# Kernel tuning notes

Hardware: AMD Instinct MI355X
Metric: run time of the kernel (lower is better)

Reference implementation:

```python
import jax, jax.numpy as jnp
import numpy as np

B, N_PATCH, DIM, HEADS = 64, 196, 768, 12
WIN = (14, 14)
NUM_REL_DIST = (2 * WIN[0] - 1) * (2 * WIN[1] - 1) + 3  # 732


def _build_rel_pos_index():
    ch, cw = np.arange(WIN[0]), np.arange(WIN[1])
    coords = np.stack(np.meshgrid(ch, cw, indexing='ij'))  # (2, Wh, Ww)
    flat = coords.reshape(2, -1)  # (2, Wh*Ww)
    rel = flat[:, :, None] - flat[:, None, :]  # (2, N, N)
    rel = rel.transpose(1, 2, 0).astype(np.int64)  # (N, N, 2)
    rel[:, :, 0] += WIN[0] - 1
    rel[:, :, 1] += WIN[1] - 1
    rel[:, :, 0] *= 2 * WIN[1] - 1
    n = WIN[0] * WIN[1] + 1
    idx = np.zeros((n, n), dtype=np.int64)
    idx[1:, 1:] = rel.sum(-1)
    idx[0, 0:] = NUM_REL_DIST - 3
    idx[0:, 0] = NUM_REL_DIST - 2
    idx[0, 0] = NUM_REL_DIST - 1
    return jnp.asarray(idx)


def setup_inputs() -> dict:
    key = jax.random.key(0)
    ks = jax.random.split(key, 6)
    d = DIM
    return {
        'x': jax.random.normal(ks[0], (B, N_PATCH + 1, d), dtype=jnp.float32),
        'qkv_w': jax.random.normal(ks[1], (3 * d, d), dtype=jnp.float32) * (d ** -0.5),
        'q_bias': jnp.zeros((d,), dtype=jnp.float32),
        'v_bias': jnp.zeros((d,), dtype=jnp.float32),
        'rpb_table': jax.random.normal(ks[2], (NUM_REL_DIST, HEADS), dtype=jnp.float32) * 0.02,
        'proj_w': jax.random.normal(ks[3], (d, d), dtype=jnp.float32) * (d ** -0.5),
        'proj_b': jnp.zeros((d,), dtype=jnp.float32),
        'rel_pos_index': _build_rel_pos_index(),
    }


def reference(x, qkv_w, q_bias, v_bias, rpb_table, proj_w, proj_b, rel_pos_index):
    Bn, N, C = x.shape
    H = HEADS
    hd = C // H
    scale = hd ** -0.5
    bias = jnp.concatenate([q_bias, jnp.zeros_like(v_bias), v_bias])
    qkv = x @ qkv_w.T + bias  # (B, N, 3C)
    qkv = qkv.reshape(Bn, N, 3, H, hd).transpose(2, 0, 3, 1, 4)  # (3, B, H, N, hd)
    q, k, v = qkv[0] * scale, qkv[1], qkv[2]
    attn = jnp.einsum('bhnd,bhmd->bhnm', q, k)  # (B, H, N, N)
    rpb = rpb_table[rel_pos_index.reshape(-1)].reshape(N, N, H).transpose(2, 0, 1)
    attn = jax.nn.softmax(attn + rpb[None], axis=-1)
    out = jnp.einsum('bhnm,bhmd->bhnd', attn, v)  # (B, H, N, hd)
    out = out.transpose(0, 2, 1, 3).reshape(Bn, N, C)
    return out @ proj_w.T + proj_b
```

## Files before the change

### kernel.cpp

```cpp
#include <hip/hip_runtime.h>
#include <hip/hip_bf16.h>

#define HEADS   12
#define HD      64
#define NTOK    197
#define BATCH   64
#define M_TOK   (BATCH*NTOK)
#define DIMC    768
#define NPAIR   (NTOK*NTOK)
#define MPAD    224

typedef __attribute__((ext_vector_type(8))) short bf16x8;
typedef __attribute__((ext_vector_type(4))) short s16x4;
typedef __attribute__((ext_vector_type(4))) float f32x4;

static __device__ __forceinline__ short f2bf(float f) {
    unsigned u = __float_as_uint(f);
    unsigned r = (u + 0x7FFFu + ((u >> 16) & 1u)) >> 16;
    return (short)r;
}

#define NX (M_TOK * DIMC)
#define NW (3 * DIMC * DIMC)
#define NP (DIMC * DIMC)
__global__ void cvt_kernel(const float* __restrict__ s0, short* __restrict__ d0,
                           const float* __restrict__ s1, short* __restrict__ d1,
                           const float* __restrict__ s2, short* __restrict__ d2) {
    int i = (blockIdx.x * 256 + threadIdx.x) * 4;
    const float* s; short* d;
    if (i < NX)                { s = s0 + i; d = d0 + i; }
    else if (i < NX + NW)      { s = s1 + (i - NX); d = d1 + (i - NX); }
    else if (i < NX + NW + NP) { s = s2 + (i - NX - NW); d = d2 + (i - NX - NW); }
    else return;
    const float4 v = *(const float4*)s;
    s16x4 b; b[0] = f2bf(v.x); b[1] = f2bf(v.y); b[2] = f2bf(v.z); b[3] = f2bf(v.w);
    *(s16x4*)d = b;
}

__global__ void rpb_kernel(const float* __restrict__ table,
                           const int* __restrict__ idx,
                           float* __restrict__ rpb_full) {
    int i = blockIdx.x * 256 + threadIdx.x;
    if (i >= NPAIR) return;
    int id = idx[i];
    #pragma unroll
    for (int h = 0; h < HEADS; ++h)
        rpb_full[(size_t)h * NPAIR + i] = table[id * HEADS + h];
}

#define STAGE(LA, LB, kt)                                                       \
    _Pragma("unroll")                                                           \
    for (int i = 0; i < 4; ++i) {                                               \
        __builtin_amdgcn_global_load_lds(                                       \
            (const __attribute__((address_space(1))) void*)(aptr[i] + (kt) * 64),\
            (__attribute__((address_space(3))) void*)&(LA)[(wv * 4 + i) * 512], \
            16, 0, 0);                                                          \
        __builtin_amdgcn_global_load_lds(                                       \
            (const __attribute__((address_space(1))) void*)(bptr[i] + (kt) * 64),\
            (__attribute__((address_space(3))) void*)&(LB)[(wv * 4 + i) * 512], \
            16, 0, 0);                                                          \
    }

#define COMPUTE(LA, LB)                                                         \
    _Pragma("unroll")                                                           \
    for (int ks = 0; ks < 2; ++ks) {                                            \
        bf16x8 af[4], bfr[4];                                                   \
        const int kk = (((ks * 4 + g) ^ (c16 & 7)) << 3);    \
        _Pragma("unroll")                                                       \
        for (int i = 0; i < 4; ++i)                                             \
            af[i] = *(const bf16x8*)&(LA)[(wr * 64 + i * 16 + c16) * 64 + kk];  \
        _Pragma("unroll")                                                       \
        for (int j = 0; j < 4; ++j)                                             \
            bfr[j] = *(const bf16x8*)&(LB)[(wc * 64 + j * 16 + c16) * 64 + kk]; \
        _Pragma("unroll")                                                       \
        for (int i = 0; i < 4; ++i)                                             \
            _Pragma("unroll")                                                   \
            for (int j = 0; j < 4; ++j)                                         \
                acc[i][j] = __builtin_amdgcn_mfma_f32_16x16x32_bf16(            \
                    af[i], bfr[j], acc[i][j], 0, 0, 0);                         \
    }

__global__ __launch_bounds__(256) void qkv_gemm_kernel(
    const short* __restrict__ xb, const short* __restrict__ wb,
    const float* __restrict__ qb, const float* __restrict__ vb,
    short* __restrict__ q_ws, short* __restrict__ k_ws,
    short* __restrict__ vt_ws) {
    __shared__ __align__(16) short lds_a0[128 * 64];
    __shared__ __align__(16) short lds_a1[128 * 64];
    __shared__ __align__(16) short lds_bb[2 * 128 * 64];
    const int tid  = threadIdx.x;
    const int lane = tid & 63;
    const int wv   = tid >> 6;
    const int wr   = wv >> 1, wc = wv & 1;
    const int flat = blockIdx.x;
    const int xcd  = flat & 7, pos = flat >> 3;
    const int swz  = ((xcd < 6) ? xcd * 223 : 1338 + (xcd - 6) * 222) + pos;
    const int bm   = swz / 18, bn = swz - bm * 18;
    const int g    = lane >> 4, c16 = lane & 15;

    f32x4 acc[4][4] = {};

    const int lrow = lane >> 3;
    const int lcol = ((lane & 7) ^ lrow) * 8;
    const short* aptr[4];
    const short* bptr[4];
    #pragma unroll
    for (int i = 0; i < 4; ++i) {
        const int r  = (wv * 4 + i) * 8 + lrow;
        int gr = bm * 128 + r; if (gr > M_TOK - 1) gr = M_TOK - 1;
        aptr[i] = xb + (size_t)gr * DIMC + lcol;
        bptr[i] = wb + (size_t)(bn * 128 + r) * DIMC + lcol;
    }

    STAGE(lds_a0, lds_bb, 0);
    __syncthreads();
    #pragma unroll
    for (int kp = 0; kp < 6; ++kp) {
        STAGE(lds_a1, (lds_bb + 8192), 2 * kp + 1);
        COMPUTE(lds_a0, lds_bb);
        __syncthreads();
        if (kp < 5) { STAGE(lds_a0, lds_bb, 2 * kp + 2); }
        COMPUTE(lds_a1, (lds_bb + 8192));
        if (kp < 5) __syncthreads();
    }

    __syncthreads();
    short* t = lds_bb;
    if (bn < 12) {
        const int isq = (bn < 6);
        #pragma unroll
        for (int j = 0; j < 4; ++j) {
            const int col = wc * 64 + j * 16 + c16;
            const int r   = isq ? bn * 128 + col : bn * 128 + col - DIMC;
            const float bias = isq ? qb[r] : 0.0f;
            #pragma unroll
            for (int i = 0; i < 4; ++i) {
                const int tok0 = wr * 64 + i * 16 + (g << 2);
                #pragma unroll
                for (int rg = 0; rg < 4; ++rg) {
                    const int tok = tok0 + rg;
                    const int sw  = ((tok >> 2) & 3) << 4;
                    float val = acc[i][j][rg];
                    if (isq) val = (val + bias) * 0.125f;
                    t[tok * 128 + (col ^ sw)] = f2bf(val);
                }
            }
        }
        __syncthreads();
        short* dst = isq ? q_ws : k_ws;
        const int rbase = isq ? bn * 128 : bn * 128 - DIMC;
        for (int tr = 0; tr < 32; ++tr) {
            const int tok = wv * 32 + tr;
            const int tt  = bm * 128 + tok;
            if (tt >= M_TOK) continue;
            const int bb = tt / NTOK, nn = tt - bb * NTOK;
            const int sw = ((tok >> 2) & 3) << 4;
            #pragma unroll
            for (int half = 0; half < 2; ++half) {
                const int col = half * 64 + lane;
                const int h   = (rbase + half * 64) >> 6;
                dst[(((size_t)bb * HEADS + h) * NTOK + nn) * HD + lane] =
                    t[tok * 128 + (col ^ sw)];
            }
        }
    } else {
        #pragma unroll
        for (int i = 0; i < 4; ++i) {
            const int lt0 = wr * 64 + i * 16 + (g << 2);
            #pragma unroll
            for (int j = 0; j < 4; ++j) {
                const int col  = wc * 64 + j * 16 + c16;
                const int sw   = (col & 7) << 3;
                const float bias = vb[(bn - 12) * 128 + col];
                #pragma unroll
                for (int rg = 0; rg < 4; ++rg)
                    t[col * 128 + ((lt0 + rg) ^ sw)] = f2bf(acc[i][j][rg] + bias);
            }
        }
        __syncthreads();
        for (int cc = 0; cc < 32; ++cc) {
            const int col = cc * 4 + wv;
            const int sw  = (col & 7) << 3;
            const int r   = bn * 128 + col - 1536;
            const int h   = r >> 6, d = r & 63;
            #pragma unroll
            for (int half = 0; half < 2; ++half) {
                const int lt = lane + half * 64;
                const int tt = bm * 128 + lt;
                if (tt < M_TOK) {
                    const int b = tt / NTOK, n = tt - b * NTOK;
                    vt_ws[(((size_t)b * HEADS + h) * HD + d) * MPAD + n] =
                        t[col * 128 + (lt ^ sw)];
                }
            }
        }
    }
}

__global__ __launch_bounds__(64) void attn_kernel(
    const short* __restrict__ q_ws, const short* __restrict__ k_ws,
    const short* __restrict__ vt_ws, const float* __restrict__ rpb_full,
    short* __restrict__ o_ws) {
    __shared__ __align__(16) short p_lds[16 * 232];
    const int lane = threadIdx.x;
    const int id   = blockIdx.x;
    const int slot = id & 7;
    const int rest = id >> 3;
    const int rt   = rest % 13;
    const int bh   = (rest / 13) * 8 + slot;
    const int b    = bh / HEADS, h = bh - b * HEADS;
    const int g    = lane >> 4, c16 = lane & 15;

    bf16x8 qa0, qa1;
    {
        const size_t base = ((size_t)bh * NTOK + (rt * 16 + c16)) * HD + g * 8;
        qa0 = *(const bf16x8*)(q_ws + base);
        qa1 = *(const bf16x8*)(q_ws + base + 32);
    }

    bf16x8 kb0[14], kb1[14];
    #pragma unroll
    for (int mt = 0; mt < 14; ++mt) {
        const size_t base = ((size_t)bh * NTOK + (mt * 16 + c16)) * HD + g * 8;
        kb0[mt] = *(const bf16x8*)(k_ws + base);
        kb1[mt] = *(const bf16x8*)(k_ws + base + 32);
    }

    f32x4 sacc[14];
    #pragma unroll
    for (int t = 0; t < 14; ++t) sacc[t] = (f32x4){0.f, 0.f, 0.f, 0.f};
    #pragma unroll
    for (int mt = 0; mt < 14; ++mt) {
        sacc[mt] = __builtin_amdgcn_mfma_f32_16x16x32_bf16(qa0, kb0[mt], sacc[mt], 0, 0, 0);
        sacc[mt] = __builtin_amdgcn_mfma_f32_16x16x32_bf16(qa1, kb1[mt], sacc[mt], 0, 0, 0);
    }

    float rp[4][14];
    #pragma unroll
    for (int rg = 0; rg < 4; ++rg) {
        int n = rt * 16 + g * 4 + rg; int nc = n > NTOK - 1 ? NTOK - 1 : n;
        const float* rbase = rpb_full + (size_t)h * NPAIR + nc * NTOK;
        #pragma unroll
        for (int mt = 0; mt < 14; ++mt) {
            int m = mt * 16 + c16; int mc = m > NTOK - 1 ? NTOK - 1 : m;
            rp[rg][mt] = rbase[mc];
        }
    }

    float mx[4] = {-1e30f, -1e30f, -1e30f, -1e30f};
    #pragma unroll
    for (int rg = 0; rg < 4; ++rg) {
        const int n = rt * 16 + g * 4 + rg;
        #pragma unroll
        for (int mt = 0; mt < 14; ++mt) {
            const int m = mt * 16 + c16;
            float s = (n < NTOK && m < NTOK) ? sacc[mt][rg] + rp[rg][mt] : -1e30f;
            sacc[mt][rg] = s;
            mx[rg] = fmaxf(mx[rg], s);
        }
    }
    #pragma unroll
    for (int off = 1; off < 16; off <<= 1)
        #pragma unroll
        for (int rg = 0; rg < 4; ++rg)
            mx[rg] = fmaxf(mx[rg], __shfl_xor(mx[rg], off, 64));

    float sm[4] = {0.f, 0.f, 0.f, 0.f};
    #pragma unroll
    for (int mt = 0; mt < 14; ++mt)
        #pragma unroll
        for (int rg = 0; rg < 4; ++rg) {
            float p = exp2f((sacc[mt][rg] - mx[rg]) * 1.44269504f);
            sm[rg] += p;
            p_lds[(g * 4 + rg) * 232 + mt * 16 + c16] = f2bf(p);
        }

    bf16x8 vbf[7][4];
    #pragma unroll
    for (int ks = 0; ks < 7; ++ks)
        #pragma unroll
        for (int j = 0; j < 4; ++j)
            vbf[ks][j] = *(const bf16x8*)(vt_ws +
                ((size_t)bh * HD + j * 16 + c16) * MPAD + ks * 32 + g * 8);

    #pragma unroll
    for (int off = 1; off < 16; off <<= 1)
        #pragma unroll
        for (int rg = 0; rg < 4; ++rg)
            sm[rg] += __shfl_xor(sm[rg], off, 64);
    __syncthreads();

    f32x4 oacc[4] = {};
    #pragma unroll
    for (int ks = 0; ks < 7; ++ks) {
        const int kk = ks * 32 + g * 8;
        bf16x8 pa = *(const bf16x8*)&p_lds[c16 * 232 + kk];
        #pragma unroll
        for (int j = 0; j < 4; ++j)
            oacc[j] = __builtin_amdgcn_mfma_f32_16x16x32_bf16(pa, vbf[ks][j], oacc[j], 0, 0, 0);
    }

    #pragma unroll
    for (int rg = 0; rg < 4; ++rg) {
        const int n = rt * 16 + g * 4 + rg;
        if (n >= NTOK) continue;
        const float inv = 1.0f / sm[rg];
        #pragma unroll
        for (int j = 0; j < 4; ++j)
            o_ws[((size_t)(b * NTOK + n)) * DIMC + h * HD + j * 16 + c16] =
                f2bf(oacc[j][rg] * inv);
    }
}

__global__ __launch_bounds__(256) void proj_gemm_kernel(
    const short* __restrict__ a, const short* __restrict__ wb,
    const float* __restrict__ pb, float* __restrict__ out) {
    __shared__ __align__(16) short lds_a0[128 * 64];
    __shared__ __align__(16) short lds_a1[128 * 64];
    __shared__ __align__(16) short lds_b0[128 * 64];
    __shared__ __align__(16) short lds_b1[128 * 64];
    const int tid  = threadIdx.x;
    const int lane = tid & 63;
    const int wv   = tid >> 6;
    const int wr   = wv >> 1, wc = wv & 1;
    const int flat = blockIdx.x;
    const int xcd  = flat & 7, pos = flat >> 3;
    const int swz  = ((xcd < 2) ? xcd * 75 : 150 + (xcd - 2) * 74) + pos;
    const int bm   = swz / 6, bn = swz - bm * 6;
    const int g    = lane >> 4, c16 = lane & 15;

    f32x4 acc[4][4] = {};

    const int lrow = lane >> 3;
    const int lcol = ((lane & 7) ^ lrow) * 8;
    const short* aptr[4];
    const short* bptr[4];
    #pragma unroll
    for (int i = 0; i < 4; ++i) {
        const int r  = (wv * 4 + i) * 8 + lrow;
        int gr = bm * 128 + r; if (gr > M_TOK - 1) gr = M_TOK - 1;
        aptr[i] = a  + (size_t)gr * DIMC + lcol;
        bptr[i] = wb + (size_t)(bn * 128 + r) * DIMC + lcol;
    }

    STAGE(lds_a0, lds_b0, 0);
    __syncthreads();
    #pragma unroll
    for (int kp = 0; kp < 6; ++kp) {
        STAGE(lds_a1, lds_b1, 2 * kp + 1);
        COMPUTE(lds_a0, lds_b0);
        __syncthreads();
        if (kp < 5) { STAGE(lds_a0, lds_b0, 2 * kp + 2); }
        COMPUTE(lds_a1, lds_b1);
        if (kp < 5) __syncthreads();
    }

    #pragma unroll
    for (int i = 0; i < 4; ++i) {
        const int tbase = bm * 128 + wr * 64 + i * 16 + (g << 2);
        #pragma unroll
        for (int j = 0; j < 4; ++j) {
            const int c   = bn * 128 + wc * 64 + j * 16 + c16;
            const float bias = pb[c];
            #pragma unroll
            for (int rg = 0; rg < 4; ++rg) {
                const int tt = tbase + rg;
                if (tt >= M_TOK) continue;
                out[(size_t)tt * DIMC + c] = acc[i][j][rg] + bias;
            }
        }
    }
}

extern "C" void kernel_launch(void* const* d_in, const int* in_sizes, int n_in,
                              void* d_out, int out_size, void* d_ws, size_t ws_size,
                              hipStream_t stream) {
    const float* x       = (const float*)d_in[0];
    const float* qkv_w   = (const float*)d_in[1];
    const float* q_bias  = (const float*)d_in[2];
    const float* v_bias  = (const float*)d_in[3];
    const float* rpb_tab = (const float*)d_in[4];
    const float* proj_w  = (const float*)d_in[5];
    const float* proj_b  = (const float*)d_in[6];
    const int*   rel_idx = (const int*)d_in[7];
    float* out = (float*)d_out;

    char* ws = (char*)d_ws;
    short* q_ws     = (short*)(ws);
    short* k_ws     = (short*)(ws + 19368192);
    short* vt_ws    = (short*)(ws + 38736384);
    short* x_bf     = (short*)(ws + 60756480);
    short* o_ws     = (short*)(ws + 60756480);
    float* rpb_full = (float*)(ws + 80122368);
    short* w_bf     = (short*)(ws + 81985200);
    short* pw_bf    = (short*)(ws + 85524144);

    const int ncvt = (NX + NW + NP) / 4;
    cvt_kernel<<<(ncvt + 255) / 256, 256, 0, stream>>>(x, x_bf, qkv_w, w_bf, proj_w, pw_bf);
    rpb_kernel<<<(NPAIR + 255) / 256, 256, 0, stream>>>(rpb_tab, rel_idx, rpb_full);

    qkv_gemm_kernel<<<1782, 256, 0, stream>>>(x_bf, w_bf, q_bias, v_bias,
                                              q_ws, k_ws, vt_ws);
    attn_kernel<<<9984, 64, 0, stream>>>(q_ws, k_ws, vt_ws, rpb_full, o_ws);
    proj_gemm_kernel<<<594, 256, 0, stream>>>(o_ws, pw_bf, proj_b, out);
}
```

Measured before the change: 185.4 us.

## Pre-layout relative position bias in bf16 lane order and coalesce attention output stores

The rpb kernel now writes the bias table in bf16, pre-arranged in the exact per-lane MFMA fragment order the attention kernel consumes, so each wave reads contiguous 64-lane chunks instead of scattered fp32 rows. The attention epilogue stages the normalized output tile through LDS and then writes full 64-element head rows per token, which replaces the strided per-fragment stores. This cuts memory traffic and improves coalescing for both the bias reads and the output writes. In exchange the bias is rounded to bf16 before it is added to the logits, and the epilogue gains two extra barriers.

After: 186.6 us. Within noise of the previous version (+0.7%).

```diff
diff --git a/kernel.cpp b/kernel.cpp
--- a/kernel.cpp
+++ b/kernel.cpp
@@ -18,6 +18,9 @@
     unsigned u = __float_as_uint(f);
     unsigned r = (u + 0x7FFFu + ((u >> 16) & 1u)) >> 16;
     return (short)r;
+}
+static __device__ __forceinline__ float bf2f(short s) {
+    return __uint_as_float(((unsigned)(unsigned short)s) << 16);
 }
 
 #define NX (M_TOK * DIMC)
@@ -37,15 +40,23 @@
     *(s16x4*)d = b;
 }
 
-__global__ void rpb_kernel(const float* __restrict__ table,
-                           const int* __restrict__ idx,
-                           float* __restrict__ rpb_full) {
+#define NRPB (HEADS * 13 * 56 * 64)
+__global__ void rpbl_kernel(const float* __restrict__ table,
+                            const int* __restrict__ idx,
+                            short* __restrict__ rpbl) {
     int i = blockIdx.x * 256 + threadIdx.x;
-    if (i >= NPAIR) return;
-    int id = idx[i];
-    #pragma unroll
-    for (int h = 0; h < HEADS; ++h)
-        rpb_full[(size_t)h * NPAIR + i] = table[id * HEADS + h];
+    if (i >= NRPB) return;
+    const int lane = i & 63;
+    const int q    = (i >> 6) % 56;
+    const int rt   = ((i >> 6) / 56) % 13;
+    const int h    = (i >> 6) / (56 * 13);
+    const int rg = q / 14, mt = q - rg * 14;
+    const int g = lane >> 4, c16 = lane & 15;
+    const int n = rt * 16 + g * 4 + rg;
+    const int m = mt * 16 + c16;
+    float v = 0.f;
+    if (n < NTOK && m < NTOK) v = table[idx[n * NTOK + m] * HEADS + h];
+    rpbl[i] = f2bf(v);
 }
 
 #define STAGE(LA, LB, kt)                                                       \
@@ -199,7 +210,7 @@
 
 __global__ __launch_bounds__(64) void attn_kernel(
     const short* __restrict__ q_ws, const short* __restrict__ k_ws,
-    const short* __restrict__ vt_ws, const float* __restrict__ rpb_full,
+    const short* __restrict__ vt_ws, const short* __restrict__ rpbL,
     short* __restrict__ o_ws) {
     __shared__ __align__(16) short p_lds[16 * 232];
     const int lane = threadIdx.x;
@@ -236,15 +247,13 @@
     }
 
     float rp[4][14];
-    #pragma unroll
-    for (int rg = 0; rg < 4; ++rg) {
-        int n = rt * 16 + g * 4 + rg; int nc = n > NTOK - 1 ? NTOK - 1 : n;
-        const float* rbase = rpb_full + (size_t)h * NPAIR + nc * NTOK;
-        #pragma unroll
-        for (int mt = 0; mt < 14; ++mt) {
-            int m = mt * 16 + c16; int mc = m > NTOK - 1 ? NTOK - 1 : m;
-            rp[rg][mt] = rbase[mc];
-        }
+    {
+        const short* rb = rpbL + (((size_t)h * 13 + rt) * 56) * 64 + lane;
+        #pragma unroll
+        for (int rg = 0; rg < 4; ++rg)
+            #pragma unroll
+            for (int mt = 0; mt < 14; ++mt)
+                rp[rg][mt] = bf2f(rb[(rg * 14 + mt) * 64]);
     }
 
     float mx[4] = {-1e30f, -1e30f, -1e30f, -1e30f};
@@ -300,15 +309,21 @@
             oacc[j] = __builtin_amdgcn_mfma_f32_16x16x32_bf16(pa, vbf[ks][j], oacc[j], 0, 0, 0);
     }
 
+    __syncthreads();
     #pragma unroll
     for (int rg = 0; rg < 4; ++rg) {
-        const int n = rt * 16 + g * 4 + rg;
-        if (n >= NTOK) continue;
         const float inv = 1.0f / sm[rg];
         #pragma unroll
         for (int j = 0; j < 4; ++j)
-            o_ws[((size_t)(b * NTOK + n)) * DIMC + h * HD + j * 16 + c16] =
-                f2bf(oacc[j][rg] * inv);
+            p_lds[(g * 4 + rg) * 72 + j * 16 + c16] = f2bf(oacc[j][rg] * inv);
+    }
+    __syncthreads();
+    const size_t obase = ((size_t)b * NTOK) * DIMC + h * HD + lane;
+    #pragma unroll
+    for (int r = 0; r < 16; ++r) {
+        const int n = rt * 16 + r;
+        if (n < NTOK)
+            o_ws[obase + (size_t)n * DIMC] = p_lds[r * 72 + lane];
     }
 }
 
@@ -391,16 +406,16 @@
     short* vt_ws    = (short*)(ws + 38736384);
     short* x_bf     = (short*)(ws + 60756480);
     short* o_ws     = (short*)(ws + 60756480);
-    float* rpb_full = (float*)(ws + 80122368);
+    short* rpbL     = (short*)(ws + 80122368);
     short* w_bf     = (short*)(ws + 81985200);
     short* pw_bf    = (short*)(ws + 85524144);
 
     const int ncvt = (NX + NW + NP) / 4;
     cvt_kernel<<<(ncvt + 255) / 256, 256, 0, stream>>>(x, x_bf, qkv_w, w_bf, proj_w, pw_bf);
-    rpb_kernel<<<(NPAIR + 255) / 256, 256, 0, stream>>>(rpb_tab, rel_idx, rpb_full);
+    rpbl_kernel<<<(NRPB + 255) / 256, 256, 0, stream>>>(rpb_tab, rel_idx, rpbL);
 
     qkv_gemm_kernel<<<1782, 256, 0, stream>>>(x_bf, w_bf, q_bias, v_bias,
                                               q_ws, k_ws, vt_ws);
-    attn_kernel<<<9984, 64, 0, stream>>>(q_ws, k_ws, vt_ws, rpb_full, o_ws);
+    attn_kernel<<<9984, 64, 0, stream>>>(q_ws, k_ws, vt_ws, rpbL, o_ws);
     proj_gemm_kernel<<<594, 256, 0, stream>>>(o_ws, pw_bf, proj_b, out);
 }
```
